# Optimization experiments

Measured on AMD Instinct MI355X. Metric: run time of the kernel, lower is better.

## Reference

```python
import jax, jax.numpy as jnp
import numpy as np

B, L, D = 8, 3072, 256
E = 4            # num_experts
K = 2            # num_experts_per_tok
H = 4 * D        # expert mlp hidden
HS = 4 * D * 1   # shared expert hidden (n_shared_experts=1)


def setup_inputs() -> dict:
    key = jax.random.key(0)
    ks = jax.random.split(key, 16)
    s = lambda *sh: 1.0 / np.sqrt(sh[0])
    return {
        "context_c": jax.random.normal(ks[0], (B, L, D), jnp.float32),
        "time_cond": jax.random.normal(ks[1], (B, D), jnp.float32),
        "gate_w": jax.random.normal(ks[2], (3 * D, E), jnp.float32) * s(3 * D),
        "gate_b": jnp.zeros((E,), jnp.float32),
        "tmod_w": jax.random.normal(ks[3], (D, 2 * E), jnp.float32) * 0.02,
        "tmod_b": jnp.zeros((2 * E,), jnp.float32),
        "ew1": jax.random.normal(ks[4], (E, D, H), jnp.float32) * s(D),
        "eb1": jnp.zeros((E, H), jnp.float32),
        "ew2": jax.random.normal(ks[5], (E, H, D), jnp.float32) * s(H),
        "eb2": jnp.zeros((E, D), jnp.float32),
        "sw1": jax.random.normal(ks[6], (D, HS), jnp.float32) * s(D),
        "sb1": jnp.zeros((HS,), jnp.float32),
        "sw2": jax.random.normal(ks[7], (HS, D), jnp.float32) * s(HS),
        "sb2": jnp.zeros((D,), jnp.float32),
    }


def reference(context_c, time_cond, gate_w, gate_b, tmod_w, tmod_b,
              ew1, eb1, ew2, eb2, sw1, sb1, sw2, sb2):
    x = context_c
    Bc, Lc, Dc = x.shape
    Lh = Lw = Lc // 3
    Lp = Lc - Lh - Lw

    # modality aggregates for gating
    head, wrist, prop = x[:, :Lh], x[:, Lh:Lh + Lw], x[:, Lh + Lw:]
    full_agg = x.mean(axis=1)
    hp_agg = (head.sum(axis=1) + prop.sum(axis=1)) / (Lh + Lp)   # mean of cat(head, proprio)
    wp_agg = (wrist.sum(axis=1) + prop.sum(axis=1)) / (Lw + Lp)  # mean of cat(wrist, proprio)
    gate_in = jnp.concatenate([full_agg, hp_agg, wp_agg], axis=-1)  # (B, 3D)

    gate_logits = gate_in @ gate_w + gate_b  # (B, E)
    # time-conditioned modulation: SiLU -> Linear -> chunk(scale, shift)
    mod = jax.nn.silu(time_cond) @ tmod_w + tmod_b
    scale, shift = jnp.split(mod, 2, axis=-1)
    gate_logits = gate_logits * (1.0 + scale) + shift

    gate_scores = jax.nn.softmax(gate_logits, axis=-1)
    topk_w, topk_i = jax.lax.top_k(gate_scores, K)
    topk_w = topk_w / (topk_w.sum(axis=-1, keepdims=True) + 1e-8)

    # dense per-expert token-wise MLP (equivalent to the gather: MLPs act per-token)
    h = jax.nn.gelu(jnp.einsum('bld,edh->belh', x, ew1) + eb1[None, :, None, :], approximate=True)
    y = jnp.einsum('belh,ehd->beld', h, ew2) + eb2[None, :, None, :]  # (B, E, L, D)

    # modality masks: expert 0 & >=3 -> all tokens; 1 -> head+proprio; 2 -> wrist+proprio
    pos = jnp.arange(Lc)
    is_head = pos < Lh
    is_wrist = (pos >= Lh) & (pos < Lh + Lw)
    is_prop = pos >= Lh + Lw
    mask = jnp.ones((E, Lc), x.dtype)
    mask = mask.at[1].set((is_head | is_prop).astype(x.dtype))
    mask = mask.at[2].set((is_wrist | is_prop).astype(x.dtype))

    # combine weights per (batch, expert) from top-k
    w_be = (jax.nn.one_hot(topk_i, E, dtype=x.dtype) * topk_w[..., None]).sum(axis=1)  # (B, E)
    out = jnp.einsum('be,beld,el->bld', w_be, y, mask)

    # shared expert
    out = out + (jax.nn.gelu(x @ sw1 + sb1, approximate=True) @ sw2 + sb2)
    return out


if __name__ == '__main__':
    o = reference(**setup_inputs())
    print(o.shape, o.dtype)
```

## Files before the change

### kernel.cpp

```cpp
#include <hip/hip_runtime.h>
#include <stdint.h>

#define Ddim 256
#define Hdim 1024
#define LSEQ 3072

typedef __bf16 bf16x8 __attribute__((ext_vector_type(8)));
typedef unsigned short u16x8 __attribute__((ext_vector_type(8)));
typedef float f32x4 __attribute__((ext_vector_type(4)));

#define MFMA(a, b, c) __builtin_amdgcn_mfma_f32_16x16x32_bf16( \
    __builtin_bit_cast(bf16x8, (a)), __builtin_bit_cast(bf16x8, (b)), (c), 0, 0, 0)

__device__ __forceinline__ unsigned short f2bf(float f) {
  unsigned int u = __float_as_uint(f);
  u = u + 0x7FFFu + ((u >> 16) & 1u);
  return (unsigned short)(u >> 16);
}

__device__ __forceinline__ float gelu_t(float x) {
  float t = 0.7978845608028654f * (x + 0.044715f * x * x * x);
  float e = __expf(2.0f * t);
  float th = 1.0f - 2.0f / (e + 1.0f);
  return 0.5f * x * (1.0f + th);
}

__device__ __forceinline__ int gate_list(const float* __restrict__ wbe, int b, int seg,
                                         int* widx, float* wsc) {
  float wv0 = wbe[b * 4 + 0], wv1 = wbe[b * 4 + 1];
  float wv2 = wbe[b * 4 + 2], wv3 = wbe[b * 4 + 3];
  int nm = 0;
  widx[nm] = 4; wsc[nm] = 1.0f; ++nm;
  if (wv0 > 0.0f) { widx[nm] = 0; wsc[nm] = wv0; ++nm; }
  if (wv1 > 0.0f && seg != 1) { widx[nm] = 1; wsc[nm] = wv1; ++nm; }
  if (wv2 > 0.0f && seg != 0) { widx[nm] = 2; wsc[nm] = wv2; ++nm; }
  if (wv3 > 0.0f && nm < 3) { widx[nm] = 3; wsc[nm] = wv3; ++nm; }
  return nm;
}

__device__ __forceinline__ void glds16(const unsigned short* g, unsigned short* l) {
  __builtin_amdgcn_global_load_lds(
      (const __attribute__((address_space(1))) unsigned int*)g,
      (__attribute__((address_space(3))) unsigned int*)l, 16, 0, 0);
}


__global__ void zero_seg(float* p) {
  p[blockIdx.x * 256 + threadIdx.x] = 0.0f;
}

__global__ void seg_reduce(const float* __restrict__ x, float* __restrict__ seg) {
  int lb = blockIdx.x, b = blockIdx.y, tid = threadIdx.x;
  const float* xg = x + ((size_t)b * LSEQ + (size_t)lb * 128) * Ddim + tid;
  float s = 0.0f;
  #pragma unroll 8
  for (int r = 0; r < 128; ++r) s += xg[(size_t)r * Ddim];
  int sg = lb >> 3;
  atomicAdd(&seg[(b * 3 + sg) * Ddim + tid], s);
}

__global__ void gate_kernel(const float* __restrict__ seg, const float* __restrict__ tc,
                            const float* __restrict__ gw, const float* __restrict__ gb,
                            const float* __restrict__ tw, const float* __restrict__ tb,
                            float* __restrict__ wbe) {
  int b = threadIdx.x >> 6, lane = threadIdx.x & 63;
  const float* sb_ = seg + b * 3 * 256;
  float pl[4] = {0.f, 0.f, 0.f, 0.f};
  for (int i = lane; i < 768; i += 64) {
    int d = i & 255, rg = i >> 8;
    float Sh = sb_[d], Sw = sb_[256 + d], Sp = sb_[512 + d];
    float val = (rg == 0) ? (Sh + Sw + Sp) * (1.0f / 3072.0f)
              : (rg == 1) ? (Sh + Sp) * (1.0f / 2048.0f)
                          : (Sw + Sp) * (1.0f / 2048.0f);
    #pragma unroll
    for (int e = 0; e < 4; ++e) pl[e] += val * gw[i * 4 + e];
  }
  float pm[8] = {0.f, 0.f, 0.f, 0.f, 0.f, 0.f, 0.f, 0.f};
  for (int d = lane; d < 256; d += 64) {
    float t = tc[b * 256 + d];
    float s = t / (1.0f + __expf(-t));
    #pragma unroll
    for (int j = 0; j < 8; ++j) pm[j] += s * tw[d * 8 + j];
  }
  #pragma unroll
  for (int off = 32; off > 0; off >>= 1) {
    #pragma unroll
    for (int e = 0; e < 4; ++e) pl[e] += __shfl_down(pl[e], off);
    #pragma unroll
    for (int j = 0; j < 8; ++j) pm[j] += __shfl_down(pm[j], off);
  }
  if (lane == 0) {
    #pragma unroll
    for (int j = 0; j < 8; ++j) pm[j] += tb[j];
    float lg[4], sc[4];
    #pragma unroll
    for (int e = 0; e < 4; ++e) lg[e] = (pl[e] + gb[e]) * (1.0f + pm[e]) + pm[4 + e];
    float mx = fmaxf(fmaxf(lg[0], lg[1]), fmaxf(lg[2], lg[3]));
    float s = 0.0f;
    #pragma unroll
    for (int e = 0; e < 4; ++e) { sc[e] = __expf(lg[e] - mx); s += sc[e]; }
    #pragma unroll
    for (int e = 0; e < 4; ++e) sc[e] /= s;
    int i1 = 0;
    #pragma unroll
    for (int e = 1; e < 4; ++e) if (sc[e] > sc[i1]) i1 = e;
    int i2 = (i1 == 0) ? 1 : 0;
    #pragma unroll
    for (int e = 0; e < 4; ++e) if (e != i1 && sc[e] > sc[i2]) i2 = e;
    float den = sc[i1] + sc[i2] + 1e-8f;
    #pragma unroll
    for (int e = 0; e < 4; ++e)
      wbe[b * 4 + e] = (e == i1) ? sc[i1] / den : ((e == i2) ? sc[i2] / den : 0.0f);
  }
}


__global__ void prep_w1f_v2(const float* __restrict__ ew1, const float* __restrict__ sw1,
                            unsigned short* __restrict__ wch) {
  int hc = blockIdx.x, id = blockIdx.y;
  const float* src = (id < 4) ? (ew1 + (size_t)id * Ddim * Hdim) : sw1;
  __shared__ float tile[256 * 33];
  int tid = threadIdx.x;
  int h0 = hc * 32;
  #pragma unroll
  for (int p = 0; p < 8; ++p) {
    int row = p * 32 + (tid >> 3);
    int c = (tid & 7) * 4;
    float4 v = *(const float4*)&src[(size_t)row * Hdim + h0 + c];
    tile[row * 33 + c] = v.x; tile[row * 33 + c + 1] = v.y;
    tile[row * 33 + c + 2] = v.z; tile[row * 33 + c + 3] = v.w;
  }
  __syncthreads();
  unsigned short* dst = wch + ((size_t)(id * 32 + hc)) * 16384;
  int lane = tid & 63, lr = lane & 15, lg = lane >> 4;
  #pragma unroll
  for (int p = 0; p < 4; ++p) {
    int f = tid + p * 256;
    int hg = (f >> 6) & 1, k = f >> 7;
    u16x8 r;
    #pragma unroll
    for (int j = 0; j < 8; ++j) r[j] = f2bf(tile[(k * 32 + lg * 8 + j) * 33 + hg * 16 + lr]);
    *(u16x8*)&dst[(size_t)f * 8] = r;
  }
}

__global__ void prep_w2f_v2(const float* __restrict__ ew2, const float* __restrict__ sw2,
                            unsigned short* __restrict__ wch) {
  int hc = blockIdx.x, id = blockIdx.y;
  const float* src = (id < 4) ? (ew2 + (size_t)id * Hdim * Ddim) : sw2;
  __shared__ float tile[32 * 264];
  int tid = threadIdx.x;
  int h0 = hc * 32;
  #pragma unroll
  for (int p = 0; p < 8; ++p) {
    int hh = p * 4 + (tid >> 6);
    int c = (tid & 63) * 4;
    float4 v = *(const float4*)&src[(size_t)(h0 + hh) * Ddim + c];
    int ci = c + (c >> 5);
    tile[hh * 264 + ci] = v.x; tile[hh * 264 + ci + 1] = v.y;
    tile[hh * 264 + ci + 2] = v.z; tile[hh * 264 + ci + 3] = v.w;
  }
  __syncthreads();
  unsigned short* dst = wch + ((size_t)(id * 32 + hc)) * 16384 + 8192;
  int lane = tid & 63, lr = lane & 15, lg = lane >> 4;
  #pragma unroll
  for (int p = 0; p < 4; ++p) {
    int f = tid + p * 256;
    int dg = f >> 6;
    u16x8 r;
    #pragma unroll
    for (int j = 0; j < 8; ++j) {
      int c = dg * 16 + lr;
      r[j] = f2bf(tile[(lg * 8 + j) * 264 + c + (c >> 5)]);
    }
    *(u16x8*)&dst[(size_t)f * 8] = r;
  }
}

__global__ __launch_bounds__(256, 2) void moe_main(
    const float* __restrict__ x, const unsigned short* __restrict__ wch,
    const float* __restrict__ eb1, const float* __restrict__ sb1,
    const float* __restrict__ eb2, const float* __restrict__ sb2,
    const float* __restrict__ wbe, float* __restrict__ out) {
  __shared__ __align__(16) unsigned short lds[2 * 16384 + 64 * 40];
  unsigned short* hid = lds + 32768;

  const int i = blockIdx.x;
  const int b = i & 7, t = i >> 3;
  const int tid = threadIdx.x;
  const int wave = tid >> 6, lane = tid & 63;
  const int lr = lane & 15, lg = lane >> 4;
  const int wm = wave >> 1, wn = wave & 1;
  const int seg = t >> 4;

  int widx[3]; float wsc[3];
  const int nm = gate_list(wbe, b, seg, widx, wsc);
  const int total = nm * 32;

  u16x8 xf[8][2];
  const float* xb = x + ((size_t)(b * LSEQ + t * 64 + wm * 32 + lr)) * Ddim;
  #pragma unroll
  for (int k = 0; k < 8; ++k) {
    #pragma unroll
    for (int mf = 0; mf < 2; ++mf) {
      const float* p = xb + (size_t)(mf * 16) * Ddim + k * 32 + lg * 8;
      float4 v0 = *(const float4*)p;
      float4 v1 = *(const float4*)(p + 4);
      u16x8 r;
      r[0] = f2bf(v0.x); r[1] = f2bf(v0.y); r[2] = f2bf(v0.z); r[3] = f2bf(v0.w);
      r[4] = f2bf(v1.x); r[5] = f2bf(v1.y); r[6] = f2bf(v1.z); r[7] = f2bf(v1.w);
      xf[k][mf] = r;
    }
  }

  f32x4 oacc[4][4];
  const f32x4 fz = {0.f, 0.f, 0.f, 0.f};
  #pragma unroll
  for (int mf = 0; mf < 4; ++mf)
    #pragma unroll
    for (int nf = 0; nf < 4; ++nf) oacc[mf][nf] = fz;

  {
    const unsigned short* src = wch + (size_t)(widx[0] * 32) * 16384 + tid * 8;
    unsigned short* l = lds + tid * 8;
    #pragma unroll
    for (int q = 0; q < 8; ++q) glds16(src + q * 2048, l + q * 2048);
  }
  __syncthreads();

  for (int j = 0; j < total; ++j) {
    unsigned short* cur = lds + (j & 1) * 16384;
    unsigned short* nxt = lds + ((j & 1) ^ 1) * 16384;

    if (j + 1 < total) {
      int m2 = (j + 1) >> 5, hc2 = (j + 1) & 31;
      const unsigned short* src = wch + (size_t)(widx[m2] * 32 + hc2) * 16384 + tid * 8;
      unsigned short* l = nxt + tid * 8;
      #pragma unroll
      for (int q = 0; q < 8; ++q) glds16(src + q * 2048, l + q * 2048);
    }

    const int m = j >> 5, hc = j & 31;
    const float* b1g = (widx[m] < 4) ? (eb1 + widx[m] * Hdim) : sb1;
    const float wscale = wsc[m];

    f32x4 a1[2];
    a1[0] = fz; a1[1] = fz;
    #pragma unroll
    for (int k = 0; k < 8; ++k) {
      u16x8 bf = *(const u16x8*)&cur[((k * 2 + wn) * 64 + lane) * 8];
      a1[0] = MFMA(xf[k][0], bf, a1[0]);
      a1[1] = MFMA(xf[k][1], bf, a1[1]);
    }
    float b1v = b1g[hc * 32 + wn * 16 + lr];
    #pragma unroll
    for (int mr = 0; mr < 2; ++mr)
      #pragma unroll
      for (int r = 0; r < 4; ++r)
        hid[(wm * 32 + mr * 16 + lg * 4 + r) * 40 + wn * 16 + lr] =
            f2bf(gelu_t(a1[mr][r] + b1v) * wscale);
    __syncthreads();

    u16x8 ha[4], wb[4];
    #pragma unroll
    for (int mf = 0; mf < 4; ++mf)
      ha[mf] = *(const u16x8*)&hid[(mf * 16 + lr) * 40 + lg * 8];
    #pragma unroll
    for (int nf = 0; nf < 4; ++nf)
      wb[nf] = *(const u16x8*)&cur[8192 + ((wave * 4 + nf) * 64 + lane) * 8];
    #pragma unroll
    for (int mf = 0; mf < 4; ++mf)
      #pragma unroll
      for (int nf = 0; nf < 4; ++nf)
        oacc[mf][nf] = MFMA(ha[mf], wb[nf], oacc[mf][nf]);
    __syncthreads();
  }

  float* og = out + ((size_t)b * LSEQ + t * 64) * Ddim;
  #pragma unroll
  for (int nf = 0; nf < 4; ++nf) {
    int dcol = wave * 64 + nf * 16 + lr;
    float bias = sb2[dcol];
    for (int m = 0; m < nm; ++m)
      if (widx[m] < 4) bias += wsc[m] * eb2[widx[m] * Ddim + dcol];
    #pragma unroll
    for (int mf = 0; mf < 4; ++mf)
      #pragma unroll
      for (int r = 0; r < 4; ++r)
        og[(size_t)(mf * 16 + lg * 4 + r) * Ddim + dcol] = oacc[mf][nf][r] + bias;
  }
}


extern "C" void kernel_launch(void* const* d_in, const int* in_sizes, int n_in,
                              void* d_out, int out_size, void* d_ws, size_t ws_size,
                              hipStream_t stream) {
  const float* x      = (const float*)d_in[0];
  const float* tc     = (const float*)d_in[1];
  const float* gate_w = (const float*)d_in[2];
  const float* gate_b = (const float*)d_in[3];
  const float* tmod_w = (const float*)d_in[4];
  const float* tmod_b = (const float*)d_in[5];
  const float* ew1    = (const float*)d_in[6];
  const float* eb1    = (const float*)d_in[7];
  const float* ew2    = (const float*)d_in[8];
  const float* eb2    = (const float*)d_in[9];
  const float* sw1    = (const float*)d_in[10];
  const float* sb1    = (const float*)d_in[11];
  const float* sw2    = (const float*)d_in[12];
  const float* sb2    = (const float*)d_in[13];
  float* out = (float*)d_out;

  char* wsb = (char*)d_ws;
  float* ws_seg = (float*)wsb;
  float* ws_wbe = (float*)(wsb + 24576);
  unsigned short* wch = (unsigned short*)(wsb + 32768);

  zero_seg<<<24, 256, 0, stream>>>(ws_seg);
  seg_reduce<<<dim3(24, 8), 256, 0, stream>>>(x, ws_seg);
  gate_kernel<<<1, 512, 0, stream>>>(ws_seg, tc, gate_w, gate_b, tmod_w, tmod_b, ws_wbe);
  prep_w1f_v2<<<dim3(32, 5), 256, 0, stream>>>(ew1, sw1, wch);
  prep_w2f_v2<<<dim3(32, 5), 256, 0, stream>>>(ew2, sw2, wch);
  moe_main<<<384, 256, 0, stream>>>(x, wch, eb1, sb1, eb2, sb2, ws_wbe, out);
}
```

Baseline: 313.2 us.

## Stream W2 fragments via registers, halve LDS, merge prep kernels and drop atomics

The main loop now stages only the W1 half of each weight chunk in LDS and loads the W2 fragments straight into registers, double-buffered across a manually unrolled pair of iterations. It also uses explicit waitcnt and barriers plus s_setprio around the MFMA blocks. Halving LDS per block could allow more resident blocks, and the register prefetch is meant to hide weight-load latency. Separately, the segment reduction writes partial sums instead of using atomics, which removes the zeroing kernel, and the two weight-prep kernels are merged into one launch. The trade-offs are higher register pressure and a stricter hand-written schedule.

```diff
diff --git a/kernel.cpp b/kernel.cpp
--- a/kernel.cpp
+++ b/kernel.cpp
@@ -23,6 +23,12 @@
   float e = __expf(2.0f * t);
   float th = 1.0f - 2.0f / (e + 1.0f);
   return 0.5f * x * (1.0f + th);
+}
+
+__device__ __forceinline__ void glds16(const unsigned short* g, unsigned short* l) {
+  __builtin_amdgcn_global_load_lds(
+      (const __attribute__((address_space(1))) unsigned int*)g,
+      (__attribute__((address_space(3))) unsigned int*)l, 16, 0, 0);
 }
 
 __device__ __forceinline__ int gate_list(const float* __restrict__ wbe, int b, int seg,
@@ -38,42 +44,36 @@
   return nm;
 }
 
-__device__ __forceinline__ void glds16(const unsigned short* g, unsigned short* l) {
-  __builtin_amdgcn_global_load_lds(
-      (const __attribute__((address_space(1))) unsigned int*)g,
-      (__attribute__((address_space(3))) unsigned int*)l, 16, 0, 0);
-}
-
-
-__global__ void zero_seg(float* p) {
-  p[blockIdx.x * 256 + threadIdx.x] = 0.0f;
-}
-
-__global__ void seg_reduce(const float* __restrict__ x, float* __restrict__ seg) {
+
+__global__ void seg_reduce(const float* __restrict__ x, float* __restrict__ part) {
   int lb = blockIdx.x, b = blockIdx.y, tid = threadIdx.x;
   const float* xg = x + ((size_t)b * LSEQ + (size_t)lb * 128) * Ddim + tid;
   float s = 0.0f;
   #pragma unroll 8
   for (int r = 0; r < 128; ++r) s += xg[(size_t)r * Ddim];
-  int sg = lb >> 3;
-  atomicAdd(&seg[(b * 3 + sg) * Ddim + tid], s);
-}
-
-__global__ void gate_kernel(const float* __restrict__ seg, const float* __restrict__ tc,
+  part[(size_t)(b * 24 + lb) * 256 + tid] = s;
+}
+
+__global__ void gate_kernel(const float* __restrict__ part, const float* __restrict__ tc,
                             const float* __restrict__ gw, const float* __restrict__ gb,
                             const float* __restrict__ tw, const float* __restrict__ tb,
                             float* __restrict__ wbe) {
   int b = threadIdx.x >> 6, lane = threadIdx.x & 63;
-  const float* sb_ = seg + b * 3 * 256;
   float pl[4] = {0.f, 0.f, 0.f, 0.f};
-  for (int i = lane; i < 768; i += 64) {
-    int d = i & 255, rg = i >> 8;
-    float Sh = sb_[d], Sw = sb_[256 + d], Sp = sb_[512 + d];
-    float val = (rg == 0) ? (Sh + Sw + Sp) * (1.0f / 3072.0f)
-              : (rg == 1) ? (Sh + Sp) * (1.0f / 2048.0f)
-                          : (Sw + Sp) * (1.0f / 2048.0f);
-    #pragma unroll
-    for (int e = 0; e < 4; ++e) pl[e] += val * gw[i * 4 + e];
+  for (int d = lane; d < 256; d += 64) {
+    float Sh = 0.f, Sw = 0.f, Sp = 0.f;
+    #pragma unroll
+    for (int lb = 0; lb < 8; ++lb)  Sh += part[(size_t)(b * 24 + lb) * 256 + d];
+    #pragma unroll
+    for (int lb = 8; lb < 16; ++lb) Sw += part[(size_t)(b * 24 + lb) * 256 + d];
+    #pragma unroll
+    for (int lb = 16; lb < 24; ++lb) Sp += part[(size_t)(b * 24 + lb) * 256 + d];
+    float vF = (Sh + Sw + Sp) * (1.0f / 3072.0f);
+    float vH = (Sh + Sp) * (1.0f / 2048.0f);
+    float vW = (Sw + Sp) * (1.0f / 2048.0f);
+    #pragma unroll
+    for (int e = 0; e < 4; ++e)
+      pl[e] += vF * gw[d * 4 + e] + vH * gw[(256 + d) * 4 + e] + vW * gw[(512 + d) * 4 + e];
   }
   float pm[8] = {0.f, 0.f, 0.f, 0.f, 0.f, 0.f, 0.f, 0.f};
   for (int d = lane; d < 256; d += 64) {
@@ -114,66 +114,61 @@
   }
 }
 
-
-__global__ void prep_w1f_v2(const float* __restrict__ ew1, const float* __restrict__ sw1,
-                            unsigned short* __restrict__ wch) {
+__global__ void prep_weights(const float* __restrict__ ew1, const float* __restrict__ sw1,
+                             const float* __restrict__ ew2, const float* __restrict__ sw2,
+                             unsigned short* __restrict__ wch) {
   int hc = blockIdx.x, id = blockIdx.y;
-  const float* src = (id < 4) ? (ew1 + (size_t)id * Ddim * Hdim) : sw1;
-  __shared__ float tile[256 * 33];
   int tid = threadIdx.x;
+  int lane = tid & 63, lr = lane & 15, lg = lane >> 4;
   int h0 = hc * 32;
-  #pragma unroll
-  for (int p = 0; p < 8; ++p) {
-    int row = p * 32 + (tid >> 3);
-    int c = (tid & 7) * 4;
-    float4 v = *(const float4*)&src[(size_t)row * Hdim + h0 + c];
-    tile[row * 33 + c] = v.x; tile[row * 33 + c + 1] = v.y;
-    tile[row * 33 + c + 2] = v.z; tile[row * 33 + c + 3] = v.w;
-  }
-  __syncthreads();
-  unsigned short* dst = wch + ((size_t)(id * 32 + hc)) * 16384;
-  int lane = tid & 63, lr = lane & 15, lg = lane >> 4;
-  #pragma unroll
-  for (int p = 0; p < 4; ++p) {
-    int f = tid + p * 256;
-    int hg = (f >> 6) & 1, k = f >> 7;
-    u16x8 r;
-    #pragma unroll
-    for (int j = 0; j < 8; ++j) r[j] = f2bf(tile[(k * 32 + lg * 8 + j) * 33 + hg * 16 + lr]);
-    *(u16x8*)&dst[(size_t)f * 8] = r;
-  }
-}
-
-__global__ void prep_w2f_v2(const float* __restrict__ ew2, const float* __restrict__ sw2,
-                            unsigned short* __restrict__ wch) {
-  int hc = blockIdx.x, id = blockIdx.y;
-  const float* src = (id < 4) ? (ew2 + (size_t)id * Hdim * Ddim) : sw2;
-  __shared__ float tile[32 * 264];
-  int tid = threadIdx.x;
-  int h0 = hc * 32;
-  #pragma unroll
-  for (int p = 0; p < 8; ++p) {
-    int hh = p * 4 + (tid >> 6);
-    int c = (tid & 63) * 4;
-    float4 v = *(const float4*)&src[(size_t)(h0 + hh) * Ddim + c];
-    int ci = c + (c >> 5);
-    tile[hh * 264 + ci] = v.x; tile[hh * 264 + ci + 1] = v.y;
-    tile[hh * 264 + ci + 2] = v.z; tile[hh * 264 + ci + 3] = v.w;
-  }
-  __syncthreads();
-  unsigned short* dst = wch + ((size_t)(id * 32 + hc)) * 16384 + 8192;
-  int lane = tid & 63, lr = lane & 15, lg = lane >> 4;
-  #pragma unroll
-  for (int p = 0; p < 4; ++p) {
-    int f = tid + p * 256;
-    int dg = f >> 6;
-    u16x8 r;
-    #pragma unroll
-    for (int j = 0; j < 8; ++j) {
-      int c = dg * 16 + lr;
-      r[j] = f2bf(tile[(lg * 8 + j) * 264 + c + (c >> 5)]);
-    }
-    *(u16x8*)&dst[(size_t)f * 8] = r;
+  if (blockIdx.z == 0) {
+    const float* src = (id < 4) ? (ew1 + (size_t)id * Ddim * Hdim) : sw1;
+    __shared__ float tile[256 * 33];
+    #pragma unroll
+    for (int p = 0; p < 8; ++p) {
+      int row = p * 32 + (tid >> 3);
+      int c = (tid & 7) * 4;
+      float4 v = *(const float4*)&src[(size_t)row * Hdim + h0 + c];
+      tile[row * 33 + c] = v.x; tile[row * 33 + c + 1] = v.y;
+      tile[row * 33 + c + 2] = v.z; tile[row * 33 + c + 3] = v.w;
+    }
+    __syncthreads();
+    unsigned short* dst = wch + ((size_t)(id * 32 + hc)) * 16384;
+    #pragma unroll
+    for (int p = 0; p < 4; ++p) {
+      int f = tid + p * 256;
+      int hg = (f >> 6) & 1, k = f >> 7;
+      u16x8 r;
+      #pragma unroll
+      for (int j = 0; j < 8; ++j) r[j] = f2bf(tile[(k * 32 + lg * 8 + j) * 33 + hg * 16 + lr]);
+      *(u16x8*)&dst[(size_t)f * 8] = r;
+    }
+  } else {
+    const float* src = (id < 4) ? (ew2 + (size_t)id * Hdim * Ddim) : sw2;
+    __shared__ float tile2[32 * 264];
+    #pragma unroll
+    for (int p = 0; p < 8; ++p) {
+      int hh = p * 4 + (tid >> 6);
+      int c = (tid & 63) * 4;
+      float4 v = *(const float4*)&src[(size_t)(h0 + hh) * Ddim + c];
+      int ci = c + (c >> 5);
+      tile2[hh * 264 + ci] = v.x; tile2[hh * 264 + ci + 1] = v.y;
+      tile2[hh * 264 + ci + 2] = v.z; tile2[hh * 264 + ci + 3] = v.w;
+    }
+    __syncthreads();
+    unsigned short* dst = wch + ((size_t)(id * 32 + hc)) * 16384 + 8192;
+    #pragma unroll
+    for (int p = 0; p < 4; ++p) {
+      int f = tid + p * 256;
+      int dg = f >> 6;
+      u16x8 r;
+      #pragma unroll
+      for (int j = 0; j < 8; ++j) {
+        int c = dg * 16 + lr;
+        r[j] = f2bf(tile2[(lg * 8 + j) * 264 + c + (c >> 5)]);
+      }
+      *(u16x8*)&dst[(size_t)f * 8] = r;
+    }
   }
 }
 
@@ -182,8 +177,10 @@
     const float* __restrict__ eb1, const float* __restrict__ sb1,
     const float* __restrict__ eb2, const float* __restrict__ sb2,
     const float* __restrict__ wbe, float* __restrict__ out) {
-  __shared__ __align__(16) unsigned short lds[2 * 16384 + 64 * 40];
-  unsigned short* hid = lds + 32768;
+  __shared__ __align__(16) unsigned short lds[2 * 8192 + 64 * 40];
+  unsigned short* const bufA = lds;
+  unsigned short* const bufB = lds + 8192;
+  unsigned short* const hid = lds + 16384;
 
   const int i = blockIdx.x;
   const int b = i & 7, t = i >> 3;
@@ -196,6 +193,9 @@
   int widx[3]; float wsc[3];
   const int nm = gate_list(wbe, b, seg, widx, wsc);
   const int total = nm * 32;
+  const int wi0 = widx[0], wi1 = (nm > 1) ? widx[1] : widx[0],
+            wi2 = (nm > 2) ? widx[2] : wi1;
+  const float sc0 = wsc[0], sc1 = (nm > 1) ? wsc[1] : 0.f, sc2 = (nm > 2) ? wsc[2] : 0.f;
 
   u16x8 xf[8][2];
   const float* xb = x + ((size_t)(b * LSEQ + t * 64 + wm * 32 + lr)) * Ddim;
@@ -220,69 +220,85 @@
     #pragma unroll
     for (int nf = 0; nf < 4; ++nf) oacc[mf][nf] = fz;
 
+  u16x8 wbA[4], wbB[4];
+
   {
-    const unsigned short* src = wch + (size_t)(widx[0] * 32) * 16384 + tid * 8;
-    unsigned short* l = lds + tid * 8;
-    #pragma unroll
-    for (int q = 0; q < 8; ++q) glds16(src + q * 2048, l + q * 2048);
-  }
-  __syncthreads();
-
-  for (int j = 0; j < total; ++j) {
-    unsigned short* cur = lds + (j & 1) * 16384;
-    unsigned short* nxt = lds + ((j & 1) ^ 1) * 16384;
-
-    if (j + 1 < total) {
-      int m2 = (j + 1) >> 5, hc2 = (j + 1) & 31;
-      const unsigned short* src = wch + (size_t)(widx[m2] * 32 + hc2) * 16384 + tid * 8;
-      unsigned short* l = nxt + tid * 8;
-      #pragma unroll
-      for (int q = 0; q < 8; ++q) glds16(src + q * 2048, l + q * 2048);
-    }
-
-    const int m = j >> 5, hc = j & 31;
-    const float* b1g = (widx[m] < 4) ? (eb1 + widx[m] * Hdim) : sb1;
-    const float wscale = wsc[m];
-
-    f32x4 a1[2];
-    a1[0] = fz; a1[1] = fz;
-    #pragma unroll
-    for (int k = 0; k < 8; ++k) {
-      u16x8 bf = *(const u16x8*)&cur[((k * 2 + wn) * 64 + lane) * 8];
-      a1[0] = MFMA(xf[k][0], bf, a1[0]);
-      a1[1] = MFMA(xf[k][1], bf, a1[1]);
-    }
-    float b1v = b1g[hc * 32 + wn * 16 + lr];
-    #pragma unroll
-    for (int mr = 0; mr < 2; ++mr)
-      #pragma unroll
-      for (int r = 0; r < 4; ++r)
-        hid[(wm * 32 + mr * 16 + lg * 4 + r) * 40 + wn * 16 + lr] =
-            f2bf(gelu_t(a1[mr][r] + b1v) * wscale);
-    __syncthreads();
-
-    u16x8 ha[4], wb[4];
-    #pragma unroll
-    for (int mf = 0; mf < 4; ++mf)
-      ha[mf] = *(const u16x8*)&hid[(mf * 16 + lr) * 40 + lg * 8];
-    #pragma unroll
-    for (int nf = 0; nf < 4; ++nf)
-      wb[nf] = *(const u16x8*)&cur[8192 + ((wave * 4 + nf) * 64 + lane) * 8];
-    #pragma unroll
-    for (int mf = 0; mf < 4; ++mf)
-      #pragma unroll
-      for (int nf = 0; nf < 4; ++nf)
-        oacc[mf][nf] = MFMA(ha[mf], wb[nf], oacc[mf][nf]);
-    __syncthreads();
-  }
+    const unsigned short* c0 = wch + (size_t)(wi0 * 32) * 16384;
+    #pragma unroll
+    for (int q = 0; q < 4; ++q) glds16(c0 + tid * 8 + q * 2048, bufA + tid * 8 + q * 2048);
+    const unsigned short* w2c = c0 + 8192 + ((size_t)(wave * 4) * 64 + lane) * 8;
+    #pragma unroll
+    for (int nf = 0; nf < 4; ++nf) wbA[nf] = *(const u16x8*)(w2c + nf * 512);
+  }
+  asm volatile("s_waitcnt vmcnt(0)" ::: "memory");
+  __builtin_amdgcn_s_barrier();
+  __builtin_amdgcn_sched_barrier(0);
+
+#define ITER(J, CUR, NXT, WBU, WBP)                                               \
+  {                                                                               \
+    const int jn = ((J) + 1 < total) ? (J) + 1 : total - 1;                       \
+    const int mN = jn >> 5, hcN = jn & 31;                                        \
+    const int idN = (mN == 0) ? wi0 : ((mN == 1) ? wi1 : wi2);                    \
+    const unsigned short* cbN = wch + (size_t)(idN * 32 + hcN) * 16384;           \
+    _Pragma("unroll")                                                             \
+    for (int q = 0; q < 4; ++q)                                                   \
+      glds16(cbN + tid * 8 + q * 2048, (NXT) + tid * 8 + q * 2048);               \
+    const unsigned short* w2n = cbN + 8192 + ((size_t)(wave * 4) * 64 + lane) * 8;\
+    _Pragma("unroll")                                                             \
+    for (int nf = 0; nf < 4; ++nf) (WBP)[nf] = *(const u16x8*)(w2n + nf * 512);   \
+    const int mC = (J) >> 5, hcC = (J) & 31;                                      \
+    const int idC = (mC == 0) ? wi0 : ((mC == 1) ? wi1 : wi2);                    \
+    const float wscale = (mC == 0) ? sc0 : ((mC == 1) ? sc1 : sc2);               \
+    const float* b1g = (idC < 4) ? (eb1 + idC * Hdim) : sb1;                      \
+    float b1v = b1g[hcC * 32 + wn * 16 + lr];                                     \
+    f32x4 a1[2]; a1[0] = fz; a1[1] = fz;                                          \
+    __builtin_amdgcn_s_setprio(1);                                                \
+    _Pragma("unroll")                                                             \
+    for (int k = 0; k < 8; ++k) {                                                 \
+      u16x8 bf = *(const u16x8*)&(CUR)[((k * 2 + wn) * 64 + lane) * 8];           \
+      a1[0] = MFMA(xf[k][0], bf, a1[0]);                                          \
+      a1[1] = MFMA(xf[k][1], bf, a1[1]);                                          \
+    }                                                                             \
+    __builtin_amdgcn_s_setprio(0);                                                \
+    _Pragma("unroll")                                                             \
+    for (int mr = 0; mr < 2; ++mr)                                                \
+      _Pragma("unroll")                                                           \
+      for (int r = 0; r < 4; ++r)                                                 \
+        hid[(wm * 32 + mr * 16 + lg * 4 + r) * 40 + wn * 16 + lr] =               \
+            f2bf(gelu_t(a1[mr][r] + b1v) * wscale);                               \
+    asm volatile("s_waitcnt lgkmcnt(0)" ::: "memory");                            \
+    __builtin_amdgcn_s_barrier();                                                 \
+    __builtin_amdgcn_sched_barrier(0);                                            \
+    u16x8 ha[4];                                                                  \
+    _Pragma("unroll")                                                             \
+    for (int mf = 0; mf < 4; ++mf)                                                \
+      ha[mf] = *(const u16x8*)&hid[(mf * 16 + lr) * 40 + lg * 8];                 \
+    __builtin_amdgcn_s_setprio(1);                                                \
+    _Pragma("unroll")                                                             \
+    for (int mf = 0; mf < 4; ++mf)                                                \
+      _Pragma("unroll")                                                           \
+      for (int nf = 0; nf < 4; ++nf)                                              \
+        oacc[mf][nf] = MFMA(ha[mf], (WBU)[nf], oacc[mf][nf]);                     \
+    __builtin_amdgcn_s_setprio(0);                                                \
+    asm volatile("s_waitcnt vmcnt(0)" ::: "memory");                              \
+    __builtin_amdgcn_s_barrier();                                                 \
+    __builtin_amdgcn_sched_barrier(0);                                            \
+  }
+
+  for (int j = 0; j < total; j += 2) {
+    ITER(j, bufA, bufB, wbA, wbB);
+    ITER(j + 1, bufB, bufA, wbB, wbA);
+  }
+#undef ITER
 
   float* og = out + ((size_t)b * LSEQ + t * 64) * Ddim;
   #pragma unroll
   for (int nf = 0; nf < 4; ++nf) {
     int dcol = wave * 64 + nf * 16 + lr;
     float bias = sb2[dcol];
-    for (int m = 0; m < nm; ++m)
-      if (widx[m] < 4) bias += wsc[m] * eb2[widx[m] * Ddim + dcol];
+    if (wi0 < 4) bias += sc0 * eb2[wi0 * Ddim + dcol];
+    if (nm > 1 && wi1 < 4) bias += sc1 * eb2[wi1 * Ddim + dcol];
+    if (nm > 2 && wi2 < 4) bias += sc2 * eb2[wi2 * Ddim + dcol];
     #pragma unroll
     for (int mf = 0; mf < 4; ++mf)
       #pragma unroll
@@ -312,14 +328,12 @@
   float* out = (float*)d_out;
 
   char* wsb = (char*)d_ws;
-  float* ws_seg = (float*)wsb;
-  float* ws_wbe = (float*)(wsb + 24576);
-  unsigned short* wch = (unsigned short*)(wsb + 32768);
-
-  zero_seg<<<24, 256, 0, stream>>>(ws_seg);
-  seg_reduce<<<dim3(24, 8), 256, 0, stream>>>(x, ws_seg);
-  gate_kernel<<<1, 512, 0, stream>>>(ws_seg, tc, gate_w, gate_b, tmod_w, tmod_b, ws_wbe);
-  prep_w1f_v2<<<dim3(32, 5), 256, 0, stream>>>(ew1, sw1, wch);
-  prep_w2f_v2<<<dim3(32, 5), 256, 0, stream>>>(ew2, sw2, wch);
+  float* ws_part = (float*)wsb;
+  float* ws_wbe  = (float*)(wsb + 200704);
+  unsigned short* wch = (unsigned short*)(wsb + 204800);
+
+  seg_reduce<<<dim3(24, 8), 256, 0, stream>>>(x, ws_part);
+  gate_kernel<<<1, 512, 0, stream>>>(ws_part, tc, gate_w, gate_b, tmod_w, tmod_b, ws_wbe);
+  prep_weights<<<dim3(32, 5, 2), 256, 0, stream>>>(ew1, sw1, ew2, sw2, wch);
   moe_main<<<384, 256, 0, stream>>>(x, wch, eb1, sb1, eb2, sb2, ws_wbe, out);
 }
```

After: 280.1 us. 1.12x faster.
